# Optimization experiments

Measured on AMD Instinct MI355X. Metric: run time of the kernel, lower is better.

Reference implementation:

```python
import jax, jax.numpy as jnp
import numpy as np

CELL_SIDE = 1.0
GRID_N = 6  # n x n occupancy grid


def _occupancy_grid(obs2):
    """Vectorized pairwise occupancy binning.
    obs2: [N, 2] -> grid [N, GRID_N*GRID_N] (counts of other pedestrians per cell)."""
    N = obs2.shape[0]
    nn = GRID_N * GRID_N
    # rel[i, j] = position of pedestrian j relative to i, in grid coords
    rel = (obs2[None, :, :] - obs2[:, None, :]) / CELL_SIDE + GRID_N / 2  # [N, N, 2]
    in_range = jnp.all((rel >= 0) & (rel < GRID_N), axis=-1)              # [N, N]
    not_self = ~jnp.eye(N, dtype=bool)
    valid = ~jnp.isnan(obs2[:, 0])                                        # [N]
    mask = in_range & not_self & valid[:, None] & valid[None, :]
    ij = jnp.clip(rel.astype(jnp.int32), 0, GRID_N - 1)                   # floor (rel>=0 under mask)
    local_bin = ij[..., 0] * GRID_N + ij[..., 1]                          # [N, N]
    # Global segment id: row i owns bins [i*nn, (i+1)*nn); invalid -> trash bin N*nn
    seg = jnp.where(mask, jnp.arange(N, dtype=jnp.int32)[:, None] * nn + local_bin, N * nn)
    counts = jax.ops.segment_sum(mask.astype(jnp.float32).reshape(-1),
                                 seg.reshape(-1), num_segments=N * nn + 1)
    return counts[: N * nn].reshape(N, nn)


def setup_inputs() -> dict:
    key = jax.random.key(0)
    k1, k2, k3, k4, k5 = jax.random.split(key, 5)
    N, hidden_dim, nn = 8192, 128, GRID_N * GRID_N
    hidden_state = jax.random.normal(k1, (N, hidden_dim), dtype=jnp.float32)
    obs1 = jax.random.normal(k2, (N, 2), dtype=jnp.float32)
    obs2 = jax.random.normal(k3, (N, 2), dtype=jnp.float32)
    W = jax.random.normal(k4, (hidden_dim, nn), dtype=jnp.float32) * (1.0 / np.sqrt(nn))
    b = jax.random.normal(k5, (hidden_dim,), dtype=jnp.float32) * 0.01
    return {"hidden_state": hidden_state, "obs1": obs1, "obs2": obs2, "W": W, "b": b}


def reference(hidden_state, obs1, obs2, W, b):
    # type_='occupancy': grid depends only on obs2; then Linear embedding.
    grid = _occupancy_grid(obs2)              # [N, 36]
    return grid @ W.T + b                     # [N, 128]
```

## Files before the change

kernel.cpp:

```cpp
#include <hip/hip_runtime.h>

#define N_PED  8192
#define HID    128
#define NN     36
#define IPB    16
#define SLICES 32
#define BLOCK  512
#define JS     256
#define HW     10
#define HPAD   3200
#define NB     512

__global__ __launch_bounds__(BLOCK, 4) void pool_kernel(
    const float* __restrict__ obs2_g,
    const float* __restrict__ Wg,
    const float* __restrict__ bias,
    float* __restrict__ out)
{
    __shared__ unsigned s_hA[HW * BLOCK + HPAD];
    __shared__ unsigned s_hB[HW * BLOCK];
    __shared__ float    s_rgrid[IPB][NN];
    __shared__ unsigned s_wsel[IPB];

    const int tid = threadIdx.x;
    const int bid = blockIdx.x;

    #pragma unroll
    for (int k = 0; k < HW; ++k) {
        s_hA[tid + k * BLOCK] = 0u;
        s_hB[tid + k * BLOCK] = 0u;
    }

    const int il    = tid & (IPB - 1);
    const int slice = tid >> 4;
    const int i     = bid * IPB + il;

    const float2 pi = ((const float2*)obs2_g)[i];
    const float  xi4 = pi.x - 4.0f;
    const float  yi4 = pi.y - 4.0f;

    if (tid < IPB) {
        float dx = pi.x - xi4;
        float dy = pi.y - yi4;
        unsigned u1 = (unsigned)((int)dx) - 1u;
        unsigned u2 = (unsigned)((int)dy) - 1u;
        bool ok = (u1 < 6u) & (u2 < 6u);
        s_wsel[il] = ok ? (u1 * 6u + u2) : 255u;
    }
    __syncthreads();

    const int tid4 = tid * 4;

    #define PAIR(H, px, py) do {                                    \
        float dx = (px) - xi4;                                      \
        float dy = (py) - yi4;                                      \
        unsigned u1 = (unsigned)((int)dx) - 1u;                     \
        unsigned u2 = (unsigned)((int)dy) - 1u;                     \
        unsigned bin = u1 * 6u + u2;                                \
        unsigned w  = ((u1 < 6u) & (u2 < 6u)) ? (bin >> 2) : 9u;    \
        unsigned sh = (bin & 3u) << 3;                              \
        H[w * BLOCK + tid] += (1u << sh);                           \
    } while (0)

    {
        const float4* jp = (const float4*)obs2_g + slice * (JS / 2);
        float4 q0 = jp[0], q1 = jp[1], q2 = jp[2], q3 = jp[3];
        for (int it = 0; it < JS / 8 - 1; ++it) {
            float4 n0 = jp[4], n1 = jp[5], n2 = jp[6], n3 = jp[7];
            jp += 4;
            PAIR(s_hA, q0.x, q0.y); PAIR(s_hB, q0.z, q0.w);
            PAIR(s_hA, q1.x, q1.y); PAIR(s_hB, q1.z, q1.w);
            PAIR(s_hA, q2.x, q2.y); PAIR(s_hB, q2.z, q2.w);
            PAIR(s_hA, q3.x, q3.y); PAIR(s_hB, q3.z, q3.w);
            q0 = n0; q1 = n1; q2 = n2; q3 = n3;
        }
        PAIR(s_hA, q0.x, q0.y); PAIR(s_hB, q0.z, q0.w);
        PAIR(s_hA, q1.x, q1.y); PAIR(s_hB, q1.z, q1.w);
        PAIR(s_hA, q2.x, q2.y); PAIR(s_hB, q2.z, q2.w);
        PAIR(s_hA, q3.x, q3.y); PAIR(s_hB, q3.z, q3.w);
    }
    #undef PAIR
    __syncthreads();

    if (tid < IPB * (HW - 1)) {
        const int ril = tid & (IPB - 1);
        const int w   = tid >> 4;
        unsigned lo = 0u, hi = 0u;
        #pragma unroll 8
        for (int sl = 0; sl < SLICES; ++sl) {
            unsigned t = sl * IPB + ril;
            unsigned a = s_hA[w * BLOCK + t];
            unsigned b = s_hB[w * BLOCK + t];
            lo += (a & 0x00FF00FFu) + (b & 0x00FF00FFu);
            hi += ((a >> 8) & 0x00FF00FFu) + ((b >> 8) & 0x00FF00FFu);
        }
        unsigned s0 = lo & 0xFFFFu;
        unsigned s1 = hi & 0xFFFFu;
        unsigned s2 = lo >> 16;
        unsigned s3 = hi >> 16;
        const unsigned sel = s_wsel[ril];
        const unsigned base = (unsigned)(w * 4);
        s0 -= (sel == base + 0u);
        s1 -= (sel == base + 1u);
        s2 -= (sel == base + 2u);
        s3 -= (sel == base + 3u);
        s_rgrid[ril][base + 0] = (float)s0;
        s_rgrid[ril][base + 1] = (float)s1;
        s_rgrid[ril][base + 2] = (float)s2;
        s_rgrid[ril][base + 3] = (float)s3;
    }
    __syncthreads();

    const int h  = tid & (HID - 1);
    const int rq = tid >> 7;
    const float4* W4 = (const float4*)Wg;

    const float bh = bias[h];
    float acc0 = bh, acc1 = bh, acc2 = bh, acc3 = bh;

    #pragma unroll
    for (int k4 = 0; k4 < 9; ++k4) {
        float4 w4 = W4[h * 9 + k4];
        float4 g0 = *(const float4*)&s_rgrid[rq     ][k4 * 4];
        float4 g1 = *(const float4*)&s_rgrid[rq +  4][k4 * 4];
        float4 g2 = *(const float4*)&s_rgrid[rq +  8][k4 * 4];
        float4 g3 = *(const float4*)&s_rgrid[rq + 12][k4 * 4];
        acc0 += g0.x * w4.x + g0.y * w4.y + g0.z * w4.z + g0.w * w4.w;
        acc1 += g1.x * w4.x + g1.y * w4.y + g1.z * w4.z + g1.w * w4.w;
        acc2 += g2.x * w4.x + g2.y * w4.y + g2.z * w4.z + g2.w * w4.w;
        acc3 += g3.x * w4.x + g3.y * w4.y + g3.z * w4.z + g3.w * w4.w;
    }

    const int obase = bid * IPB;
    out[(obase + rq     ) * HID + h] = acc0;
    out[(obase + rq +  4) * HID + h] = acc1;
    out[(obase + rq +  8) * HID + h] = acc2;
    out[(obase + rq + 12) * HID + h] = acc3;
}

extern "C" void kernel_launch(void* const* d_in, const int* in_sizes, int n_in,
                              void* d_out, int out_size, void* d_ws, size_t ws_size,
                              hipStream_t stream) {
    const float* obs2 = (const float*)d_in[2];
    const float* W    = (const float*)d_in[3];
    const float* b    = (const float*)d_in[4];
    float* out        = (float*)d_out;
    (void)in_sizes; (void)n_in; (void)out_size; (void)d_ws; (void)ws_size;

    hipLaunchKernelGGL(pool_kernel, dim3(NB), dim3(BLOCK), 0, stream,
                       obs2, W, b, out);
}
```

Measured before the change: 41.44 us.

## Halve pedestrians per block, drop trash histogram row, raise occupancy

Each block now handles 8 pedestrians instead of 16 across 64 slices of 128 neighbours, doubling the grid to 1024 blocks. The trash word row and padding are removed from the shared histograms. Out-of-range pairs now add zero to word 0 instead of writing to a discard row. Launch bounds ask for 8 blocks per CU, aiming to cut shared memory per block and raise occupancy. The cost is more blocks re-reading all of obs2 and fewer output rows per block in the GEMV stage.

Measured after the change: 43.01 us. +3.8%, slower.

```diff
diff --git a/kernel.cpp b/kernel.cpp
--- a/kernel.cpp
+++ b/kernel.cpp
@@ -3,22 +3,21 @@
 #define N_PED  8192
 #define HID    128
 #define NN     36
-#define IPB    16
-#define SLICES 32
+#define IPB    8
+#define SLICES 64
 #define BLOCK  512
-#define JS     256
-#define HW     10
-#define HPAD   3200
-#define NB     512
+#define JS     128
+#define HWW    9
+#define NB     1024
 
-__global__ __launch_bounds__(BLOCK, 4) void pool_kernel(
+__global__ __launch_bounds__(BLOCK, 8) void pool_kernel(
     const float* __restrict__ obs2_g,
     const float* __restrict__ Wg,
     const float* __restrict__ bias,
     float* __restrict__ out)
 {
-    __shared__ unsigned s_hA[HW * BLOCK + HPAD];
-    __shared__ unsigned s_hB[HW * BLOCK];
+    __shared__ unsigned s_hA[HWW * BLOCK];
+    __shared__ unsigned s_hB[HWW * BLOCK];
     __shared__ float    s_rgrid[IPB][NN];
     __shared__ unsigned s_wsel[IPB];
 
@@ -26,13 +25,13 @@
     const int bid = blockIdx.x;
 
     #pragma unroll
-    for (int k = 0; k < HW; ++k) {
+    for (int k = 0; k < HWW; ++k) {
         s_hA[tid + k * BLOCK] = 0u;
         s_hB[tid + k * BLOCK] = 0u;
     }
 
     const int il    = tid & (IPB - 1);
-    const int slice = tid >> 4;
+    const int slice = tid >> 3;
     const int i     = bid * IPB + il;
 
     const float2 pi = ((const float2*)obs2_g)[i];
@@ -49,17 +48,17 @@
     }
     __syncthreads();
 
-    const int tid4 = tid * 4;
-
     #define PAIR(H, px, py) do {                                    \
         float dx = (px) - xi4;                                      \
         float dy = (py) - yi4;                                      \
         unsigned u1 = (unsigned)((int)dx) - 1u;                     \
         unsigned u2 = (unsigned)((int)dy) - 1u;                     \
+        unsigned mx = u1 > u2 ? u1 : u2;                            \
+        bool ok = mx < 6u;                                          \
         unsigned bin = u1 * 6u + u2;                                \
-        unsigned w  = ((u1 < 6u) & (u2 < 6u)) ? (bin >> 2) : 9u;    \
-        unsigned sh = (bin & 3u) << 3;                              \
-        H[w * BLOCK + tid] += (1u << sh);                           \
+        unsigned w   = ok ? (bin >> 2) : 0u;                        \
+        unsigned inc = ok ? (1u << ((bin & 3u) << 3)) : 0u;         \
+        H[w * BLOCK + tid] += inc;                                  \
     } while (0)
 
     {
@@ -82,9 +81,9 @@
     #undef PAIR
     __syncthreads();
 
-    if (tid < IPB * (HW - 1)) {
+    if (tid < IPB * HWW) {
         const int ril = tid & (IPB - 1);
-        const int w   = tid >> 4;
+        const int w   = tid >> 3;
         unsigned lo = 0u, hi = 0u;
         #pragma unroll 8
         for (int sl = 0; sl < SLICES; ++sl) {
@@ -98,7 +97,7 @@
         unsigned s1 = hi & 0xFFFFu;
         unsigned s2 = lo >> 16;
         unsigned s3 = hi >> 16;
-        const unsigned sel = s_wsel[ril];
+        const unsigned sel  = s_wsel[ril];
         const unsigned base = (unsigned)(w * 4);
         s0 -= (sel == base + 0u);
         s1 -= (sel == base + 1u);
@@ -112,30 +111,24 @@
     __syncthreads();
 
     const int h  = tid & (HID - 1);
-    const int rq = tid >> 7;
+    const int r0 = tid >> 7;
     const float4* W4 = (const float4*)Wg;
 
     const float bh = bias[h];
-    float acc0 = bh, acc1 = bh, acc2 = bh, acc3 = bh;
+    float acc0 = bh, acc1 = bh;
 
     #pragma unroll
     for (int k4 = 0; k4 < 9; ++k4) {
         float4 w4 = W4[h * 9 + k4];
-        float4 g0 = *(const float4*)&s_rgrid[rq     ][k4 * 4];
-        float4 g1 = *(const float4*)&s_rgrid[rq +  4][k4 * 4];
-        float4 g2 = *(const float4*)&s_rgrid[rq +  8][k4 * 4];
-        float4 g3 = *(const float4*)&s_rgrid[rq + 12][k4 * 4];
+        float4 g0 = *(const float4*)&s_rgrid[r0    ][k4 * 4];
+        float4 g1 = *(const float4*)&s_rgrid[r0 + 4][k4 * 4];
         acc0 += g0.x * w4.x + g0.y * w4.y + g0.z * w4.z + g0.w * w4.w;
         acc1 += g1.x * w4.x + g1.y * w4.y + g1.z * w4.z + g1.w * w4.w;
-        acc2 += g2.x * w4.x + g2.y * w4.y + g2.z * w4.z + g2.w * w4.w;
-        acc3 += g3.x * w4.x + g3.y * w4.y + g3.z * w4.z + g3.w * w4.w;
     }
 
     const int obase = bid * IPB;
-    out[(obase + rq     ) * HID + h] = acc0;
-    out[(obase + rq +  4) * HID + h] = acc1;
-    out[(obase + rq +  8) * HID + h] = acc2;
-    out[(obase + rq + 12) * HID + h] = acc3;
+    out[(obase + r0    ) * HID + h] = acc0;
+    out[(obase + r0 + 4) * HID + h] = acc1;
 }
 
 extern "C" void kernel_launch(void* const* d_in, const int* in_sizes, int n_in,
```
